# Kernel optimization log

Hardware: AMD Instinct MI355X
Metric: run time of the kernel (lower is better)

## Reference

```python
import jax, jax.numpy as jnp
import numpy as np

N, FDIM, HDIM, STEPS = 8192, 512, 1024, 50
STRESS, QNOISE = 0.0, 0.1


def setup_inputs() -> dict:
    key = jax.random.key(0)
    ks = jax.random.split(key, 20)
    s = 0.02
    d = {
        "real_antigen": jax.random.normal(ks[0], (N, FDIM), jnp.float32),
        "steps": STEPS,
        # quantum gene projection (self-loop graph -> per-node linear)
        "Wq": jax.random.normal(ks[1], (FDIM, HDIM), jnp.float32) * s,
        "bq": jnp.zeros((HDIM,), jnp.float32),
        # denoise_0: Linear(h,h) ReLU Linear(h,f)
        "W01": jax.random.normal(ks[2], (HDIM, HDIM), jnp.float32) * s,
        "b01": jnp.zeros((HDIM,), jnp.float32),
        "W02": jax.random.normal(ks[3], (HDIM, FDIM), jnp.float32) * s,
        "b02": jnp.zeros((FDIM,), jnp.float32),
        # denoise_1: Linear(h,h) Tanh Linear(h,f)
        "W11": jax.random.normal(ks[4], (HDIM, HDIM), jnp.float32) * s,
        "b11": jnp.zeros((HDIM,), jnp.float32),
        "W12": jax.random.normal(ks[5], (HDIM, FDIM), jnp.float32) * s,
        "b12": jnp.zeros((FDIM,), jnp.float32),
        # interference_net: Linear(2f,h) GELU Linear(h,f)
        "Wi1": jax.random.normal(ks[6], (2 * FDIM, HDIM), jnp.float32) * s,
        "bi1": jnp.zeros((HDIM,), jnp.float32),
        "Wi2": jax.random.normal(ks[7], (HDIM, FDIM), jnp.float32) * s,
        "bi2": jnp.zeros((FDIM,), jnp.float32),
        # quantum state scalars
        "alpha_amp": jnp.asarray(np.cos(0.6), jnp.float32),
        "beta_amp": jnp.asarray(np.sin(0.6), jnp.float32),
        "phase_cos": jnp.asarray(np.cos(0.3), jnp.float32),
    }
    return d


def reference(real_antigen, steps, Wq, bq, W01, b01, W02, b02, W11, b11,
              W12, b12, Wi1, bi1, Wi2, bi2, alpha_amp, beta_amp, phase_cos):
    sched = jnp.linspace(1e-4, 0.02, 100, dtype=jnp.float32)
    decoherence_rate = jnp.float32(0.1 + STRESS * 0.5)
    decay = jnp.exp(-decoherence_rate)
    # quantum probabilities (fixed amplitudes during the rollout)
    a2, b2 = alpha_amp ** 2, beta_amp ** 2
    p0 = a2 / (a2 + b2)
    p1 = b2 / (a2 + b2)
    sp0, sp1 = jnp.sqrt(p0), jnp.sqrt(p1)
    base_key = jax.random.key(1)
    x0 = jax.random.normal(jax.random.fold_in(base_key, 10_000), real_antigen.shape, jnp.float32)

    def step(carry, t):
        x, coh = carry
        qf = jax.nn.relu(x @ Wq + bq)                           # [N, H]
        d0 = jax.nn.relu(qf @ W01 + b01) @ W02 + b02            # [N, F]
        d1 = jnp.tanh(qf @ W11 + b11) @ W12 + b12               # [N, F]
        inter_in = jnp.concatenate([d0, d1], axis=-1)           # [N, 2F]
        interf = jax.nn.gelu(inter_in @ Wi1 + bi1, approximate=False) @ Wi2 + bi2
        qi = 2.0 * jnp.sqrt(p0 * p1) * phase_cos * coh          # scalar interference
        denoised = sp0 * d0 + sp1 * d1 + qi * interf
        alpha = jnp.maximum(1.0 - sched[t], 1e-8)
        alpha_prev = jnp.where(t > 0, 1.0 - sched[jnp.maximum(t - 1, 0)], 1.0)
        sqrt_1ma = jnp.sqrt(jnp.maximum(1.0 - alpha, 1e-8))
        x_new = (x - (1.0 - alpha) / sqrt_1ma * denoised) / jnp.sqrt(alpha)
        sigma = jnp.sqrt(jnp.maximum((1.0 - alpha_prev) / (1.0 - alpha) * (1.0 - alpha / alpha_prev), 0.0))
        noise = jax.random.normal(jax.random.fold_in(base_key, t), x.shape, jnp.float32)
        x_new = jnp.where(t > 0, x_new + (sigma + QNOISE * jnp.abs(qi)) * noise, x_new)
        return (x_new, coh * decay), None

    ts = jnp.arange(int(steps) - 1, -1, -1, dtype=jnp.int32)
    (x, _), _ = jax.lax.scan(step, (x0, jnp.float32(1.0)), ts)
    # quantum measurement: collapse to |0> with probability p0
    u = jax.random.uniform(jax.random.fold_in(base_key, 99_999), (), jnp.float32)
    dream = jnp.where(u < p0, 0.7 * x + 0.3 * real_antigen, x)
    return dream
```

## Files before the change

kernel.cpp:

```cpp
#include <hip/hip_runtime.h>
#include <stdint.h>
#include <math.h>


typedef __bf16 bf16x8 __attribute__((ext_vector_type(8)));
typedef float floatx4 __attribute__((ext_vector_type(4)));

__host__ __device__ inline void tf2x32(uint32_t k0, uint32_t k1,
                                       uint32_t x0, uint32_t x1,
                                       uint32_t& o0, uint32_t& o1) {
  uint32_t ks2 = k0 ^ k1 ^ 0x1BD11BDAu;
#define TF_R(r) { x0 += x1; x1 = (x1 << (r)) | (x1 >> (32 - (r))); x1 ^= x0; }
  x0 += k0; x1 += k1;
  TF_R(13) TF_R(15) TF_R(26) TF_R(6)
  x0 += k1;  x1 += ks2 + 1u;
  TF_R(17) TF_R(29) TF_R(16) TF_R(24)
  x0 += ks2; x1 += k0 + 2u;
  TF_R(13) TF_R(15) TF_R(26) TF_R(6)
  x0 += k0;  x1 += k1 + 3u;
  TF_R(17) TF_R(29) TF_R(16) TF_R(24)
  x0 += k1;  x1 += ks2 + 4u;
  TF_R(13) TF_R(15) TF_R(26) TF_R(6)
  x0 += ks2; x1 += k0 + 5u;
#undef TF_R
  o0 = x0; o1 = x1;
}

__device__ inline float erfinv_f32(float x) {
  float w = -log1pf(-x * x);
  float p;
  if (w < 5.0f) {
    w = w - 2.5f;
    p = 2.81022636e-08f;
    p = fmaf(p, w, 3.43273939e-07f);
    p = fmaf(p, w, -3.5233877e-06f);
    p = fmaf(p, w, -4.39150654e-06f);
    p = fmaf(p, w, 0.00021858087f);
    p = fmaf(p, w, -0.00125372503f);
    p = fmaf(p, w, -0.00417768164f);
    p = fmaf(p, w, 0.246640727f);
    p = fmaf(p, w, 1.50140941f);
  } else {
    w = sqrtf(w) - 3.0f;
    p = -0.000200214257f;
    p = fmaf(p, w, 0.000100950558f);
    p = fmaf(p, w, 0.00134934322f);
    p = fmaf(p, w, -0.00367342844f);
    p = fmaf(p, w, 0.00573950773f);
    p = fmaf(p, w, -0.0076224613f);
    p = fmaf(p, w, 0.00943887047f);
    p = fmaf(p, w, 1.00167406f);
    p = fmaf(p, w, 2.83297682f);
  }
  return p * x;
}

__device__ inline float tf_normal(uint32_t k0, uint32_t k1, uint32_t i) {
  uint32_t o0, o1;
  tf2x32(k0, k1, 0u, i, o0, o1);
  uint32_t bits = o0 ^ o1;
  float f = __uint_as_float(0x3F800000u | (bits >> 9)) - 1.0f;
  float u = f * 2.0f + (-0.99999994f);
  u = fmaxf(-0.99999994f, u);
  return 1.41421356f * erfinv_f32(u);
}

__device__ inline unsigned short f2bf(float f) {
  uint32_t u = __float_as_uint(f);
  u += 0x7FFFu + ((u >> 16) & 1u);
  return (unsigned short)(u >> 16);
}
__device__ inline float bf2f(unsigned short h) {
  return __uint_as_float(((uint32_t)h) << 16);
}

__global__ __launch_bounds__(256)
void transpose_bf16_kernel(const float* __restrict__ W,
                           unsigned short* __restrict__ Wt, int K, int N) {
  __shared__ float tile[32][33];
  int kb = blockIdx.x * 32, nb = blockIdx.y * 32;
  int tx = threadIdx.x & 31, ty = threadIdx.x >> 5;
#pragma unroll
  for (int i = 0; i < 32; i += 8)
    tile[ty + i][tx] = W[(size_t)(kb + ty + i) * N + nb + tx];
  __syncthreads();
#pragma unroll
  for (int i = 0; i < 32; i += 8)
    Wt[(size_t)(nb + ty + i) * K + kb + tx] = f2bf(tile[tx][ty + i]);
}

template<int MH, int NH>
__device__ __forceinline__ void phase_mfma8(bf16x8 (&a)[4][2], bf16x8 (&b)[4][2],
                                            floatx4 (&acc)[8][4]) {
  asm volatile("s_waitcnt lgkmcnt(0)" ::: "memory");
  __builtin_amdgcn_sched_barrier(0);
  __builtin_amdgcn_s_setprio(1);
#pragma unroll
  for (int s = 0; s < 2; s++)
#pragma unroll
    for (int mm = 0; mm < 4; mm++)
#pragma unroll
      for (int nn = 0; nn < 2; nn++)
        acc[MH * 4 + mm][NH * 2 + nn] = __builtin_amdgcn_mfma_f32_16x16x32_bf16(
            a[mm][s], b[NH * 2 + nn][s], acc[MH * 4 + mm][NH * 2 + nn], 0, 0, 0);
  __builtin_amdgcn_s_setprio(0);
}

template<int MH, int NH>
__device__ __forceinline__ void phase_mfma4(bf16x8 (&a)[4][2], bf16x8 (&b)[4][2],
                                            floatx4 (&acc)[4][4]) {
  asm volatile("s_waitcnt lgkmcnt(0)" ::: "memory");
  __builtin_amdgcn_sched_barrier(0);
  __builtin_amdgcn_s_setprio(1);
#pragma unroll
  for (int s = 0; s < 2; s++)
#pragma unroll
    for (int mm = 0; mm < 2; mm++)
#pragma unroll
      for (int nn = 0; nn < 2; nn++)
        acc[MH * 2 + mm][NH * 2 + nn] = __builtin_amdgcn_mfma_f32_16x16x32_bf16(
            a[MH * 2 + mm][s], b[NH * 2 + nn][s], acc[MH * 2 + mm][NH * 2 + nn],
            0, 0, 0);
  __builtin_amdgcn_s_setprio(0);
}

template<int ACT, int PAIR>
__global__ __launch_bounds__(512, 2)
void mfma_gemm_8ph_128x256(const unsigned short* __restrict__ A0,
                           const unsigned short* __restrict__ A1,
                           int lda0, int lda1, int K0, int Ktot,
                           const unsigned short* __restrict__ Bt,
                           const float* __restrict__ bias,
                           unsigned short* __restrict__ C, int ldc,
                           const unsigned short* __restrict__ Ab,
                           const unsigned short* __restrict__ Btb,
                           const float* __restrict__ biasb,
                           unsigned short* __restrict__ Cb) {
  __shared__ unsigned short As[2][128 * 64];
  __shared__ unsigned short Bs[2][256 * 64];
  const int tid = threadIdx.x;
  const int wave = tid >> 6, lane = tid & 63;
  const int wr = wave >> 2, wc = wave & 3;
  const int fm = lane & 15, quad = lane >> 4;
  const int id = blockIdx.x;
  const int nid = (id & 7) * 32 + (id >> 3);
  int row0, col0;
  if (PAIR) {
    const int rem = nid & 127;
    row0 = (rem & 63) << 7;
    col0 = (rem >> 6) << 8;
    if (nid >> 7) { A0 = Ab; A1 = Ab; Bt = Btb; bias = biasb; C = Cb; }
  } else {
    row0 = (nid & 63) << 7;
    col0 = (nid >> 6) << 8;
  }
  const int NKT = Ktot >> 6;

  auto stageA = [&](int tile, int buf, int h) {
    if (tile >= NKT) return;
    const int kk = tile << 6;
    const unsigned short* Ap; int kOff, lda;
    if (kk < K0) { Ap = A0; kOff = kk; lda = lda0; }
    else         { Ap = A1; kOff = kk - K0; lda = lda1; }
    const int sr = tid >> 3, gc = tid & 7;
    __builtin_amdgcn_global_load_lds(
        (const __attribute__((address_space(1))) uint32_t*)
            (Ap + (size_t)(row0 + h * 64 + sr) * lda + kOff + ((gc ^ (sr & 7)) << 3)),
        (__attribute__((address_space(3))) uint32_t*)(&As[buf][h * 4096 + tid * 8]),
        16, 0, 0);
  };
  auto stageB = [&](int tile, int buf, int h) {
    if (tile >= NKT) return;
    const int kk = tile << 6;
#pragma unroll
    for (int c = 0; c < 2; c++) {
      int g2 = c * 512 + tid;
      int sr = g2 >> 3, gc = g2 & 7;
      __builtin_amdgcn_global_load_lds(
          (const __attribute__((address_space(1))) uint32_t*)
              (Bt + (size_t)(col0 + h * 128 + sr) * Ktot + kk + ((gc ^ (sr & 7)) << 3)),
          (__attribute__((address_space(3))) uint32_t*)(&Bs[buf][h * 8192 + g2 * 8]),
          16, 0, 0);
    }
  };

  const int aswz = (fm & 7) << 3;
  auto rdA = [&](int buf, int m, int s) {
    return *(const bf16x8*)(&As[buf][(wr * 64 + m * 16 + fm) * 64 +
                                     ((s * 32 + quad * 8) ^ aswz)]);
  };
  auto rdB = [&](int buf, int n, int s) {
    return *(const bf16x8*)(&Bs[buf][(wc * 64 + n * 16 + fm) * 64 +
                                     ((s * 32 + quad * 8) ^ aswz)]);
  };

  floatx4 acc[4][4];
#pragma unroll
  for (int m = 0; m < 4; m++)
#pragma unroll
    for (int n = 0; n < 4; n++) acc[m][n] = (floatx4){0.f, 0.f, 0.f, 0.f};

  stageA(0, 0, 0); stageA(0, 0, 1);
  stageB(0, 0, 0); stageB(0, 0, 1);
  stageB(1, 1, 0); stageB(1, 1, 1);
  asm volatile("s_waitcnt vmcnt(4)" ::: "memory");
  asm volatile("s_barrier" ::: "memory");

  const int NJ = NKT >> 1;
#pragma unroll 1
  for (int j = 0; j < NJ; j++) {
    const int t1 = 2 * j + 1;
    bf16x8 a[4][2], b[4][2];
#pragma unroll
    for (int mm = 0; mm < 2; mm++) { a[mm][0] = rdA(0, mm, 0); a[mm][1] = rdA(0, mm, 1); }
#pragma unroll
    for (int nn = 0; nn < 2; nn++) { b[nn][0] = rdB(0, nn, 0); b[nn][1] = rdB(0, nn, 1); }
    stageA(t1, 1, 0);
    asm volatile("s_barrier" ::: "memory");
    phase_mfma4<0, 0>(a, b, acc);
    asm volatile("s_barrier" ::: "memory");
#pragma unroll
    for (int nn = 2; nn < 4; nn++) { b[nn][0] = rdB(0, nn, 0); b[nn][1] = rdB(0, nn, 1); }
    stageA(t1, 1, 1);
    asm volatile("s_barrier" ::: "memory");
    phase_mfma4<0, 1>(a, b, acc);
    asm volatile("s_barrier" ::: "memory");
#pragma unroll
    for (int mm = 2; mm < 4; mm++) { a[mm][0] = rdA(0, mm, 0); a[mm][1] = rdA(0, mm, 1); }
    stageB(t1 + 1, 0, 0);
    asm volatile("s_barrier" ::: "memory");
    phase_mfma4<1, 1>(a, b, acc);
    asm volatile("s_barrier" ::: "memory");
    stageB(t1 + 1, 0, 1);
    asm volatile("s_barrier" ::: "memory");
    phase_mfma4<1, 0>(a, b, acc);
    if (j == NJ - 1) asm volatile("s_waitcnt vmcnt(0)" ::: "memory");
    else             asm volatile("s_waitcnt vmcnt(4)" ::: "memory");
    asm volatile("s_barrier" ::: "memory");
#pragma unroll
    for (int mm = 0; mm < 2; mm++) { a[mm][0] = rdA(1, mm, 0); a[mm][1] = rdA(1, mm, 1); }
#pragma unroll
    for (int nn = 0; nn < 2; nn++) { b[nn][0] = rdB(1, nn, 0); b[nn][1] = rdB(1, nn, 1); }
    stageA(t1 + 1, 0, 0);
    asm volatile("s_barrier" ::: "memory");
    phase_mfma4<0, 0>(a, b, acc);
    asm volatile("s_barrier" ::: "memory");
#pragma unroll
    for (int nn = 2; nn < 4; nn++) { b[nn][0] = rdB(1, nn, 0); b[nn][1] = rdB(1, nn, 1); }
    stageA(t1 + 1, 0, 1);
    asm volatile("s_barrier" ::: "memory");
    phase_mfma4<0, 1>(a, b, acc);
    asm volatile("s_barrier" ::: "memory");
#pragma unroll
    for (int mm = 2; mm < 4; mm++) { a[mm][0] = rdA(1, mm, 0); a[mm][1] = rdA(1, mm, 1); }
    stageB(t1 + 2, 1, 0);
    asm volatile("s_barrier" ::: "memory");
    phase_mfma4<1, 1>(a, b, acc);
    asm volatile("s_barrier" ::: "memory");
    stageB(t1 + 2, 1, 1);
    asm volatile("s_barrier" ::: "memory");
    phase_mfma4<1, 0>(a, b, acc);
    asm volatile("s_waitcnt vmcnt(4)" ::: "memory");
    asm volatile("s_barrier" ::: "memory");
  }

#pragma unroll
  for (int n = 0; n < 4; n++) {
    int col = col0 + wc * 64 + n * 16 + fm;
    float bv = bias[col];
#pragma unroll
    for (int m = 0; m < 4; m++) {
      int rbase = row0 + wr * 64 + m * 16 + quad * 4;
#pragma unroll
      for (int r = 0; r < 4; r++) {
        float val = acc[m][n][r] + bv;
        if (ACT == 1) val = fmaxf(val, 0.0f);
        if (ACT == 3) val = 0.5f * val * (1.0f + erff(val * 0.70710678118654752f));
        C[(size_t)(rbase + r) * ldc + col] = f2bf(val);
      }
    }
  }
}

__global__ __launch_bounds__(512, 2)
void mfma_gemm2_8ph(const unsigned short* __restrict__ A,
                    const unsigned short* __restrict__ Bt,
                    const float* __restrict__ bias0,
                    const float* __restrict__ bias1,
                    unsigned short* __restrict__ C0,
                    unsigned short* __restrict__ C1) {
  constexpr int NKT = 16;
  __shared__ unsigned short As[2][256 * 64];
  __shared__ unsigned short Bs[2][256 * 64];
  const int tid = threadIdx.x;
  const int wave = tid >> 6, lane = tid & 63;
  const int wr = wave >> 2, wc = wave & 3;
  const int fm = lane & 15, quad = lane >> 4;
  const int id = blockIdx.x;
  const int nid = (id & 7) * 32 + (id >> 3);
  const int row0 = (nid & 31) << 8;
  const int col0 = (nid >> 5) << 8;

  auto stageA = [&](int tile, int buf, int h) {
    if (tile >= NKT) return;
    const int kk = tile << 6;
#pragma unroll
    for (int c = 0; c < 2; c++) {
      int g2 = c * 512 + tid;
      int sr = g2 >> 3, gc = g2 & 7;
      __builtin_amdgcn_global_load_lds(
          (const __attribute__((address_space(1))) uint32_t*)
              (A + (size_t)(row0 + h * 128 + sr) * 1024 + kk + ((gc ^ (sr & 7)) << 3)),
          (__attribute__((address_space(3))) uint32_t*)(&As[buf][h * 8192 + g2 * 8]),
          16, 0, 0);
    }
  };
  auto stageB = [&](int tile, int buf, int h) {
    if (tile >= NKT) return;
    const int kk = tile << 6;
#pragma unroll
    for (int c = 0; c < 2; c++) {
      int g2 = c * 512 + tid;
      int sr = g2 >> 3, gc = g2 & 7;
      __builtin_amdgcn_global_load_lds(
          (const __attribute__((address_space(1))) uint32_t*)
              (Bt + (size_t)(col0 + h * 128 + sr) * 1024 + kk + ((gc ^ (sr & 7)) << 3)),
          (__attribute__((address_space(3))) uint32_t*)(&Bs[buf][h * 8192 + g2 * 8]),
          16, 0, 0);
    }
  };

  const int aswz = (fm & 7) << 3;
  auto rdA = [&](int buf, int m, int s) {
    return *(const bf16x8*)(&As[buf][(wr * 128 + m * 16 + fm) * 64 +
                                     ((s * 32 + quad * 8) ^ aswz)]);
  };
  auto rdB = [&](int buf, int n, int s) {
    return *(const bf16x8*)(&Bs[buf][(wc * 64 + n * 16 + fm) * 64 +
                                     ((s * 32 + quad * 8) ^ aswz)]);
  };

  floatx4 acc[8][4];
#pragma unroll
  for (int m = 0; m < 8; m++)
#pragma unroll
    for (int n = 0; n < 4; n++) acc[m][n] = (floatx4){0.f, 0.f, 0.f, 0.f};

  stageA(0, 0, 0); stageA(0, 0, 1);
  stageB(0, 0, 0); stageB(0, 0, 1);
  stageB(1, 1, 0); stageB(1, 1, 1);
  asm volatile("s_waitcnt vmcnt(4)" ::: "memory");
  asm volatile("s_barrier" ::: "memory");

#pragma unroll 1
  for (int j = 0; j < 8; j++) {
    const int t1 = 2 * j + 1;
    bf16x8 a[4][2], b[4][2];
#pragma unroll
    for (int mm = 0; mm < 4; mm++) { a[mm][0] = rdA(0, mm, 0); a[mm][1] = rdA(0, mm, 1); }
#pragma unroll
    for (int nn = 0; nn < 2; nn++) { b[nn][0] = rdB(0, nn, 0); b[nn][1] = rdB(0, nn, 1); }
    stageA(t1, 1, 0);
    asm volatile("s_barrier" ::: "memory");
    phase_mfma8<0, 0>(a, b, acc);
    asm volatile("s_barrier" ::: "memory");
#pragma unroll
    for (int nn = 2; nn < 4; nn++) { b[nn][0] = rdB(0, nn, 0); b[nn][1] = rdB(0, nn, 1); }
    stageA(t1, 1, 1);
    asm volatile("s_barrier" ::: "memory");
    phase_mfma8<0, 1>(a, b, acc);
    asm volatile("s_barrier" ::: "memory");
#pragma unroll
    for (int mm = 0; mm < 4; mm++) { a[mm][0] = rdA(0, 4 + mm, 0); a[mm][1] = rdA(0, 4 + mm, 1); }
    stageB(t1 + 1, 0, 0);
    asm volatile("s_barrier" ::: "memory");
    phase_mfma8<1, 1>(a, b, acc);
    asm volatile("s_barrier" ::: "memory");
    stageB(t1 + 1, 0, 1);
    asm volatile("s_barrier" ::: "memory");
    phase_mfma8<1, 0>(a, b, acc);
    if (j == 7) asm volatile("s_waitcnt vmcnt(0)" ::: "memory");
    else        asm volatile("s_waitcnt vmcnt(4)" ::: "memory");
    asm volatile("s_barrier" ::: "memory");
#pragma unroll
    for (int mm = 0; mm < 4; mm++) { a[mm][0] = rdA(1, mm, 0); a[mm][1] = rdA(1, mm, 1); }
#pragma unroll
    for (int nn = 0; nn < 2; nn++) { b[nn][0] = rdB(1, nn, 0); b[nn][1] = rdB(1, nn, 1); }
    stageA(t1 + 1, 0, 0);
    asm volatile("s_barrier" ::: "memory");
    phase_mfma8<0, 0>(a, b, acc);
    asm volatile("s_barrier" ::: "memory");
#pragma unroll
    for (int nn = 2; nn < 4; nn++) { b[nn][0] = rdB(1, nn, 0); b[nn][1] = rdB(1, nn, 1); }
    stageA(t1 + 1, 0, 1);
    asm volatile("s_barrier" ::: "memory");
    phase_mfma8<0, 1>(a, b, acc);
    asm volatile("s_barrier" ::: "memory");
#pragma unroll
    for (int mm = 0; mm < 4; mm++) { a[mm][0] = rdA(1, 4 + mm, 0); a[mm][1] = rdA(1, 4 + mm, 1); }
    stageB(t1 + 2, 1, 0);
    asm volatile("s_barrier" ::: "memory");
    phase_mfma8<1, 1>(a, b, acc);
    asm volatile("s_barrier" ::: "memory");
    stageB(t1 + 2, 1, 1);
    asm volatile("s_barrier" ::: "memory");
    phase_mfma8<1, 0>(a, b, acc);
    asm volatile("s_waitcnt vmcnt(4)" ::: "memory");
    asm volatile("s_barrier" ::: "memory");
  }

  const bool side = (col0 >= 1024);
  const float* bias = side ? bias1 : bias0;
  unsigned short* C = side ? C1 : C0;
  const int cb = col0 - (side ? 1024 : 0);
#pragma unroll
  for (int n = 0; n < 4; n++) {
    int col = cb + wc * 64 + n * 16 + fm;
    float bv = bias[col];
#pragma unroll
    for (int m = 0; m < 8; m++) {
      int rbase = row0 + wr * 128 + m * 16 + quad * 4;
#pragma unroll
      for (int r = 0; r < 4; r++) {
        float val = acc[m][n][r] + bv;
        val = side ? tanhf(val) : fmaxf(val, 0.0f);
        C[(size_t)(rbase + r) * 1024 + col] = f2bf(val);
      }
    }
  }
}

__global__ __launch_bounds__(512, 4)
void mfma_gemm_update(const unsigned short* __restrict__ A,
                      const unsigned short* __restrict__ Bt,
                      const float* __restrict__ bias,
                      const unsigned short* __restrict__ d0,
                      const unsigned short* __restrict__ d1,
                      float* __restrict__ x,
                      unsigned short* __restrict__ xbf,
                      const float* __restrict__ a_amp,
                      const float* __restrict__ b_amp,
                      const float* __restrict__ ph,
                      float coh, float c1, float sqa, float sigma,
                      int add_noise, uint32_t k0, uint32_t k1) {
  __shared__ unsigned short As[2][64 * 32];
  __shared__ unsigned short Bs[2][128 * 32];
  const int tid = threadIdx.x;
  const int wave = tid >> 6, lane = tid & 63;
  const int wr = wave >> 2, wc = wave & 3;
  const int fm = lane & 15, quad = lane >> 4;
  const int id = blockIdx.x + gridDim.x * blockIdx.y;
  const int row0 = (id & 127) << 6;
  const int col0 = (id >> 7) << 7;
  const int sArow = (tid & 255) >> 2;
  const int sBrow = tid >> 2;
  const int sgr = (tid & 3) * 8;

  auto issue = [&](int kt, int buf) {
    const int kk = kt * 32;
    __builtin_amdgcn_global_load_lds(
        (const __attribute__((address_space(1))) uint32_t*)
            (A + (size_t)(row0 + sArow) * 1024 + kk + sgr),
        (__attribute__((address_space(3))) uint32_t*)(&As[buf][sArow * 32 + sgr]),
        16, 0, 0);
    __builtin_amdgcn_global_load_lds(
        (const __attribute__((address_space(1))) uint32_t*)
            (Bt + (size_t)(col0 + sBrow) * 1024 + kk + sgr),
        (__attribute__((address_space(3))) uint32_t*)(&Bs[buf][sBrow * 32 + sgr]),
        16, 0, 0);
  };

  floatx4 acc[2][2];
#pragma unroll
  for (int tm = 0; tm < 2; tm++)
#pragma unroll
    for (int tn = 0; tn < 2; tn++) acc[tm][tn] = (floatx4){0.f, 0.f, 0.f, 0.f};

  const int nk = 32;
  issue(0, 0);
  for (int k = 0; k < nk; k++) {
    const int cur = k & 1;
    if (k + 1 < nk) {
      issue(k + 1, cur ^ 1);
      asm volatile("s_waitcnt vmcnt(2)\ns_barrier" ::: "memory");
    } else {
      asm volatile("s_waitcnt vmcnt(0)\ns_barrier" ::: "memory");
    }
    bf16x8 a[2], b[2];
#pragma unroll
    for (int tm = 0; tm < 2; tm++)
      a[tm] = *(const bf16x8*)(&As[cur][(wr * 32 + tm * 16 + fm) * 32 + quad * 8]);
#pragma unroll
    for (int tn = 0; tn < 2; tn++)
      b[tn] = *(const bf16x8*)(&Bs[cur][(wc * 32 + tn * 16 + fm) * 32 + quad * 8]);
#pragma unroll
    for (int tm = 0; tm < 2; tm++)
#pragma unroll
      for (int tn = 0; tn < 2; tn++)
        acc[tm][tn] = __builtin_amdgcn_mfma_f32_16x16x32_bf16(a[tm], b[tn],
                                                              acc[tm][tn], 0, 0, 0);
    asm volatile("s_barrier" ::: "memory");
  }

  float aa = a_amp[0], bb = b_amp[0], pc = ph[0];
  float a2 = aa * aa, b2 = bb * bb, s = a2 + b2;
  float p0 = a2 / s, p1 = b2 / s;
  float sp0 = sqrtf(p0), sp1 = sqrtf(p1);
  float qi = 2.0f * sqrtf(p0 * p1) * pc * coh;
  float nscale = sigma + 0.1f * fabsf(qi);

#pragma unroll
  for (int tn = 0; tn < 2; tn++) {
    int col = col0 + wc * 32 + tn * 16 + fm;
    float bv = bias[col];
#pragma unroll
    for (int tm = 0; tm < 2; tm++) {
      int rbase = row0 + wr * 32 + tm * 16 + quad * 4;
#pragma unroll
      for (int r = 0; r < 4; r++) {
        int row = rbase + r;
        size_t i = (size_t)row * 512 + col;
        float itf = acc[tm][tn][r] + bv;
        float den = sp0 * bf2f(d0[i]) + sp1 * bf2f(d1[i]) + qi * itf;
        float xn = (x[i] - c1 * den) / sqa;
        if (add_noise) xn += nscale * tf_normal(k0, k1, (uint32_t)i);
        x[i] = xn;
        xbf[i] = f2bf(xn);
      }
    }
  }
}

__global__ void init_normal_kernel(float* __restrict__ x,
                                   unsigned short* __restrict__ xbf,
                                   uint32_t k0, uint32_t k1, int n) {
  int i = blockIdx.x * blockDim.x + threadIdx.x;
  if (i >= n) return;
  float v = tf_normal(k0, k1, (uint32_t)i);
  x[i] = v;
  xbf[i] = f2bf(v);
}

__global__ void final_kernel(const float* __restrict__ x,
                             const float* __restrict__ real,
                             float* __restrict__ out,
                             const float* __restrict__ a_amp,
                             const float* __restrict__ b_amp,
                             uint32_t k0, uint32_t k1, int n) {
  int i = blockIdx.x * blockDim.x + threadIdx.x;
  if (i >= n) return;
  float aa = a_amp[0], bb = b_amp[0];
  float a2 = aa * aa, b2 = bb * bb;
  float p0 = a2 / (a2 + b2);
  uint32_t o0, o1;
  tf2x32(k0, k1, 0u, 0u, o0, o1);
  uint32_t bits = o0 ^ o1;
  float u = __uint_as_float(0x3F800000u | (bits >> 9)) - 1.0f;
  float xv = x[i];
  out[i] = (u < p0) ? (0.7f * xv + 0.3f * real[i]) : xv;
}

extern "C" void kernel_launch(void* const* d_in, const int* in_sizes, int n_in,
                              void* d_out, int out_size, void* d_ws,
                              size_t ws_size, hipStream_t stream) {
  const float* real = (const float*)d_in[0];
  const float* Wq  = (const float*)d_in[2];
  const float* bq  = (const float*)d_in[3];
  const float* W01 = (const float*)d_in[4];
  const float* b01 = (const float*)d_in[5];
  const float* W02 = (const float*)d_in[6];
  const float* b02 = (const float*)d_in[7];
  const float* W11 = (const float*)d_in[8];
  const float* b11 = (const float*)d_in[9];
  const float* W12 = (const float*)d_in[10];
  const float* b12 = (const float*)d_in[11];
  const float* Wi1 = (const float*)d_in[12];
  const float* bi1 = (const float*)d_in[13];
  const float* Wi2 = (const float*)d_in[14];
  const float* bi2 = (const float*)d_in[15];
  const float* a_amp = (const float*)d_in[16];
  const float* b_amp = (const float*)d_in[17];
  const float* ph    = (const float*)d_in[18];

  const int Nn = 8192, F = 512, H = 1024;
  const int nElem = Nn * F;

  char* ws = (char*)d_ws;
  float* x = (float*)ws;                                   ws += (size_t)nElem * 4;
  unsigned short* xbf = (unsigned short*)ws;               ws += (size_t)nElem * 2;
  unsigned short* qf  = (unsigned short*)ws;               ws += (size_t)Nn * H * 2;
  unsigned short* h0  = (unsigned short*)ws;               ws += (size_t)Nn * H * 2;
  unsigned short* h1  = (unsigned short*)ws;               ws += (size_t)Nn * H * 2;
  unsigned short* d0  = (unsigned short*)ws;               ws += (size_t)nElem * 2;
  unsigned short* d1  = (unsigned short*)ws;               ws += (size_t)nElem * 2;
  unsigned short* Wq_t  = (unsigned short*)ws;             ws += (size_t)F * H * 2;
  unsigned short* WA_t  = (unsigned short*)ws;             ws += (size_t)(2 * H) * H * 2;
  unsigned short* W02_t = (unsigned short*)ws;             ws += (size_t)H * F * 2;
  unsigned short* W12_t = (unsigned short*)ws;             ws += (size_t)H * F * 2;
  unsigned short* Wi1_t = (unsigned short*)ws;             ws += (size_t)(2 * F) * H * 2;
  unsigned short* Wi2_t = (unsigned short*)ws;             ws += (size_t)H * F * 2;

  dim3 tb(256);
  transpose_bf16_kernel<<<dim3(F / 32, H / 32), tb, 0, stream>>>(Wq, Wq_t, F, H);
  transpose_bf16_kernel<<<dim3(H / 32, H / 32), tb, 0, stream>>>(W01, WA_t, H, H);
  transpose_bf16_kernel<<<dim3(H / 32, H / 32), tb, 0, stream>>>(W11, WA_t + (size_t)H * H, H, H);
  transpose_bf16_kernel<<<dim3(H / 32, F / 32), tb, 0, stream>>>(W02, W02_t, H, F);
  transpose_bf16_kernel<<<dim3(H / 32, F / 32), tb, 0, stream>>>(W12, W12_t, H, F);
  transpose_bf16_kernel<<<dim3(2 * F / 32, H / 32), tb, 0, stream>>>(Wi1, Wi1_t, 2 * F, H);
  transpose_bf16_kernel<<<dim3(H / 32, F / 32), tb, 0, stream>>>(Wi2, Wi2_t, H, F);

  uint32_t kx0, kx1; tf2x32(0u, 1u, 0u, 10000u, kx0, kx1);
  init_normal_kernel<<<(nElem + 255) / 256, 256, 0, stream>>>(x, xbf, kx0, kx1, nElem);

  float sched[100];
  for (int i = 0; i < 100; i++)
    sched[i] = (float)(1e-4 + (0.02 - 1e-4) * (double)i / 99.0);
  const float decay = expf(-0.1f);
  float coh = 1.0f;

  dim3 blk(512);
  dim3 g8(256);
  dim3 g7(F / 128, Nn / 64);

  for (int j = 0; j < 50; j++) {
    int t = 49 - j;
    mfma_gemm_8ph_128x256<1, 0><<<g8, blk, 0, stream>>>(
        xbf, xbf, F, F, F, F, Wq_t, bq, qf, H,
        nullptr, nullptr, nullptr, nullptr);
    mfma_gemm2_8ph<<<g8, blk, 0, stream>>>(qf, WA_t, b01, b11, h0, h1);
    mfma_gemm_8ph_128x256<0, 1><<<g8, blk, 0, stream>>>(
        h0, h0, H, H, H, H, W02_t, b02, d0, F,
        h1, W12_t, b12, d1);
    mfma_gemm_8ph_128x256<3, 0><<<g8, blk, 0, stream>>>(
        d0, d1, F, F, F, 2 * F, Wi1_t, bi1, qf, H,
        nullptr, nullptr, nullptr, nullptr);

    float schedt = sched[t];
    float alphaf = fmaxf(1.0f - schedt, 1e-8f);
    float one_m_alpha = 1.0f - alphaf;
    float sqrt_1ma = sqrtf(fmaxf(one_m_alpha, 1e-8f));
    float c1 = one_m_alpha / sqrt_1ma;
    float sqa = sqrtf(alphaf);
    float sigma = 0.0f;
    if (t > 0) {
      float ap = 1.0f - sched[t - 1];
      sigma = sqrtf(fmaxf((1.0f - ap) / one_m_alpha * (1.0f - alphaf / ap), 0.0f));
    }
    uint32_t kt0, kt1; tf2x32(0u, 1u, 0u, (uint32_t)t, kt0, kt1);
    mfma_gemm_update<<<g7, blk, 0, stream>>>(
        qf, Wi2_t, bi2, d0, d1, x, xbf, a_amp, b_amp, ph, coh, c1, sqa, sigma,
        (t > 0) ? 1 : 0, kt0, kt1);
    coh *= decay;
  }

  uint32_t ku0, ku1; tf2x32(0u, 1u, 0u, 99999u, ku0, ku1);
  final_kernel<<<(nElem + 255) / 256, 256, 0, stream>>>(
      x, real, (float*)d_out, a_amp, b_amp, ku0, ku1, nElem);
}
```

Measured before the change: 8.053 ms.

## Shrink generic GEMM tile to 128x128 with 512 blocks; batch weight transposes

The generic 8-phase MFMA GEMM goes from a 128x256 to a 128x128 output tile. Each wave now holds a 4x2 accumulator set, the B staging buffer is halved, and launch bounds allow 4 blocks per CU. The grid doubles to 512 blocks so the three GEMMs using this kernel fill the 256 CUs more evenly and can hide latency with higher occupancy, at the cost of less B-operand reuse per block and more A re-reads. The seven weight-transpose launches are also merged into one batched kernel indexed by blockIdx.z, which cuts launch overhead in setup.

```diff
diff --git a/kernel.cpp b/kernel.cpp
--- a/kernel.cpp
+++ b/kernel.cpp
@@ -74,11 +74,22 @@
   return __uint_as_float(((uint32_t)h) << 16);
 }
 
+struct TPBatch {
+  const float* W[7];
+  unsigned short* Wt[7];
+  int K[7];
+  int N[7];
+};
+
 __global__ __launch_bounds__(256)
-void transpose_bf16_kernel(const float* __restrict__ W,
-                           unsigned short* __restrict__ Wt, int K, int N) {
+void transpose_bf16_batched(TPBatch tp) {
+  const int z = blockIdx.z;
+  const int K = tp.K[z], N = tp.N[z];
+  const int kb = blockIdx.x * 32, nb = blockIdx.y * 32;
+  if (kb >= K || nb >= N) return;
+  const float* __restrict__ W = tp.W[z];
+  unsigned short* __restrict__ Wt = tp.Wt[z];
   __shared__ float tile[32][33];
-  int kb = blockIdx.x * 32, nb = blockIdx.y * 32;
   int tx = threadIdx.x & 31, ty = threadIdx.x >> 5;
 #pragma unroll
   for (int i = 0; i < 32; i += 8)
@@ -107,8 +118,8 @@
 }
 
 template<int MH, int NH>
-__device__ __forceinline__ void phase_mfma4(bf16x8 (&a)[4][2], bf16x8 (&b)[4][2],
-                                            floatx4 (&acc)[4][4]) {
+__device__ __forceinline__ void phase_mfma2(bf16x8 (&a)[4][2], bf16x8 (&b)[2][2],
+                                            floatx4 (&acc)[4][2]) {
   asm volatile("s_waitcnt lgkmcnt(0)" ::: "memory");
   __builtin_amdgcn_sched_barrier(0);
   __builtin_amdgcn_s_setprio(1);
@@ -116,17 +127,14 @@
   for (int s = 0; s < 2; s++)
 #pragma unroll
     for (int mm = 0; mm < 2; mm++)
-#pragma unroll
-      for (int nn = 0; nn < 2; nn++)
-        acc[MH * 2 + mm][NH * 2 + nn] = __builtin_amdgcn_mfma_f32_16x16x32_bf16(
-            a[MH * 2 + mm][s], b[NH * 2 + nn][s], acc[MH * 2 + mm][NH * 2 + nn],
-            0, 0, 0);
+      acc[MH * 2 + mm][NH] = __builtin_amdgcn_mfma_f32_16x16x32_bf16(
+          a[MH * 2 + mm][s], b[NH][s], acc[MH * 2 + mm][NH], 0, 0, 0);
   __builtin_amdgcn_s_setprio(0);
 }
 
 template<int ACT, int PAIR>
-__global__ __launch_bounds__(512, 2)
-void mfma_gemm_8ph_128x256(const unsigned short* __restrict__ A0,
+__global__ __launch_bounds__(512, 4)
+void mfma_gemm_8ph_128x128(const unsigned short* __restrict__ A0,
                            const unsigned short* __restrict__ A1,
                            int lda0, int lda1, int K0, int Ktot,
                            const unsigned short* __restrict__ Bt,
@@ -137,22 +145,22 @@
                            const float* __restrict__ biasb,
                            unsigned short* __restrict__ Cb) {
   __shared__ unsigned short As[2][128 * 64];
-  __shared__ unsigned short Bs[2][256 * 64];
+  __shared__ unsigned short Bs[2][128 * 64];
   const int tid = threadIdx.x;
   const int wave = tid >> 6, lane = tid & 63;
   const int wr = wave >> 2, wc = wave & 3;
   const int fm = lane & 15, quad = lane >> 4;
   const int id = blockIdx.x;
-  const int nid = (id & 7) * 32 + (id >> 3);
+  const int nid = (id & 7) * 64 + (id >> 3);
   int row0, col0;
   if (PAIR) {
-    const int rem = nid & 127;
+    const int rem = nid & 255;
     row0 = (rem & 63) << 7;
-    col0 = (rem >> 6) << 8;
-    if (nid >> 7) { A0 = Ab; A1 = Ab; Bt = Btb; bias = biasb; C = Cb; }
+    col0 = (rem >> 6) << 7;
+    if (nid >> 8) { A0 = Ab; A1 = Ab; Bt = Btb; bias = biasb; C = Cb; }
   } else {
     row0 = (nid & 63) << 7;
-    col0 = (nid >> 6) << 8;
+    col0 = (nid >> 6) << 7;
   }
   const int NKT = Ktot >> 6;
 
@@ -172,16 +180,12 @@
   auto stageB = [&](int tile, int buf, int h) {
     if (tile >= NKT) return;
     const int kk = tile << 6;
-#pragma unroll
-    for (int c = 0; c < 2; c++) {
-      int g2 = c * 512 + tid;
-      int sr = g2 >> 3, gc = g2 & 7;
-      __builtin_amdgcn_global_load_lds(
-          (const __attribute__((address_space(1))) uint32_t*)
-              (Bt + (size_t)(col0 + h * 128 + sr) * Ktot + kk + ((gc ^ (sr & 7)) << 3)),
-          (__attribute__((address_space(3))) uint32_t*)(&Bs[buf][h * 8192 + g2 * 8]),
-          16, 0, 0);
-    }
+    const int sr = tid >> 3, gc = tid & 7;
+    __builtin_amdgcn_global_load_lds(
+        (const __attribute__((address_space(1))) uint32_t*)
+            (Bt + (size_t)(col0 + h * 64 + sr) * Ktot + kk + ((gc ^ (sr & 7)) << 3)),
+        (__attribute__((address_space(3))) uint32_t*)(&Bs[buf][h * 4096 + tid * 8]),
+        16, 0, 0);
   };
 
   const int aswz = (fm & 7) << 3;
@@ -190,83 +194,79 @@
                                      ((s * 32 + quad * 8) ^ aswz)]);
   };
   auto rdB = [&](int buf, int n, int s) {
-    return *(const bf16x8*)(&Bs[buf][(wc * 64 + n * 16 + fm) * 64 +
+    return *(const bf16x8*)(&Bs[buf][(wc * 32 + n * 16 + fm) * 64 +
                                      ((s * 32 + quad * 8) ^ aswz)]);
   };
 
-  floatx4 acc[4][4];
+  floatx4 acc[4][2];
 #pragma unroll
   for (int m = 0; m < 4; m++)
 #pragma unroll
-    for (int n = 0; n < 4; n++) acc[m][n] = (floatx4){0.f, 0.f, 0.f, 0.f};
+    for (int n = 0; n < 2; n++) acc[m][n] = (floatx4){0.f, 0.f, 0.f, 0.f};
 
   stageA(0, 0, 0); stageA(0, 0, 1);
   stageB(0, 0, 0); stageB(0, 0, 1);
   stageB(1, 1, 0); stageB(1, 1, 1);
-  asm volatile("s_waitcnt vmcnt(4)" ::: "memory");
+  asm volatile("s_waitcnt vmcnt(2)" ::: "memory");
   asm volatile("s_barrier" ::: "memory");
 
   const int NJ = NKT >> 1;
 #pragma unroll 1
   for (int j = 0; j < NJ; j++) {
     const int t1 = 2 * j + 1;
-    bf16x8 a[4][2], b[4][2];
+    bf16x8 a[4][2], b[2][2];
 #pragma unroll
     for (int mm = 0; mm < 2; mm++) { a[mm][0] = rdA(0, mm, 0); a[mm][1] = rdA(0, mm, 1); }
-#pragma unroll
-    for (int nn = 0; nn < 2; nn++) { b[nn][0] = rdB(0, nn, 0); b[nn][1] = rdB(0, nn, 1); }
+    b[0][0] = rdB(0, 0, 0); b[0][1] = rdB(0, 0, 1);
     stageA(t1, 1, 0);
     asm volatile("s_barrier" ::: "memory");
-    phase_mfma4<0, 0>(a, b, acc);
-    asm volatile("s_barrier" ::: "memory");
-#pragma unroll
-    for (int nn = 2; nn < 4; nn++) { b[nn][0] = rdB(0, nn, 0); b[nn][1] = rdB(0, nn, 1); }
+    phase_mfma2<0, 0>(a, b, acc);
+    asm volatile("s_barrier" ::: "memory");
+    b[1][0] = rdB(0, 1, 0); b[1][1] = rdB(0, 1, 1);
     stageA(t1, 1, 1);
     asm volatile("s_barrier" ::: "memory");
-    phase_mfma4<0, 1>(a, b, acc);
+    phase_mfma2<0, 1>(a, b, acc);
     asm volatile("s_barrier" ::: "memory");
 #pragma unroll
     for (int mm = 2; mm < 4; mm++) { a[mm][0] = rdA(0, mm, 0); a[mm][1] = rdA(0, mm, 1); }
     stageB(t1 + 1, 0, 0);
     asm volatile("s_barrier" ::: "memory");
-    phase_mfma4<1, 1>(a, b, acc);
+    phase_mfma2<1, 1>(a, b, acc);
     asm volatile("s_barrier" ::: "memory");
     stageB(t1 + 1, 0, 1);
     asm volatile("s_barrier" ::: "memory");
-    phase_mfma4<1, 0>(a, b, acc);
+    phase_mfma2<1, 0>(a, b, acc);
     if (j == NJ - 1) asm volatile("s_waitcnt vmcnt(0)" ::: "memory");
-    else             asm volatile("s_waitcnt vmcnt(4)" ::: "memory");
+    else             asm volatile("s_waitcnt vmcnt(2)" ::: "memory");
     asm volatile("s_barrier" ::: "memory");
 #pragma unroll
     for (int mm = 0; mm < 2; mm++) { a[mm][0] = rdA(1, mm, 0); a[mm][1] = rdA(1, mm, 1); }
-#pragma unroll
-    for (int nn = 0; nn < 2; nn++) { b[nn][0] = rdB(1, nn, 0); b[nn][1] = rdB(1, nn, 1); }
+    b[0][0] = rdB(1, 0, 0); b[0][1] = rdB(1, 0, 1);
     stageA(t1 + 1, 0, 0);
     asm volatile("s_barrier" ::: "memory");
-    phase_mfma4<0, 0>(a, b, acc);
-    asm volatile("s_barrier" ::: "memory");
-#pragma unroll
-    for (int nn = 2; nn < 4; nn++) { b[nn][0] = rdB(1, nn, 0); b[nn][1] = rdB(1, nn, 1); }
+    phase_mfma2<0, 0>(a, b, acc);
+    asm volatile("s_barrier" ::: "memory");
+    b[1][0] = rdB(1, 1, 0); b[1][1] = rdB(1, 1, 1);
     stageA(t1 + 1, 0, 1);
     asm volatile("s_barrier" ::: "memory");
-    phase_mfma4<0, 1>(a, b, acc);
+    phase_mfma2<0, 1>(a, b, acc);
     asm volatile("s_barrier" ::: "memory");
 #pragma unroll
     for (int mm = 2; mm < 4; mm++) { a[mm][0] = rdA(1, mm, 0); a[mm][1] = rdA(1, mm, 1); }
     stageB(t1 + 2, 1, 0);
     asm volatile("s_barrier" ::: "memory");
-    phase_mfma4<1, 1>(a, b, acc);
+    phase_mfma2<1, 1>(a, b, acc);
     asm volatile("s_barrier" ::: "memory");
     stageB(t1 + 2, 1, 1);
     asm volatile("s_barrier" ::: "memory");
-    phase_mfma4<1, 0>(a, b, acc);
-    asm volatile("s_waitcnt vmcnt(4)" ::: "memory");
-    asm volatile("s_barrier" ::: "memory");
-  }
-
-#pragma unroll
-  for (int n = 0; n < 4; n++) {
-    int col = col0 + wc * 64 + n * 16 + fm;
+    phase_mfma2<1, 0>(a, b, acc);
+    asm volatile("s_waitcnt vmcnt(2)" ::: "memory");
+    asm volatile("s_barrier" ::: "memory");
+  }
+
+#pragma unroll
+  for (int n = 0; n < 2; n++) {
+    int col = col0 + wc * 32 + n * 16 + fm;
     float bv = bias[col];
 #pragma unroll
     for (int m = 0; m < 4; m++) {
@@ -600,14 +600,15 @@
   unsigned short* Wi1_t = (unsigned short*)ws;             ws += (size_t)(2 * F) * H * 2;
   unsigned short* Wi2_t = (unsigned short*)ws;             ws += (size_t)H * F * 2;
 
-  dim3 tb(256);
-  transpose_bf16_kernel<<<dim3(F / 32, H / 32), tb, 0, stream>>>(Wq, Wq_t, F, H);
-  transpose_bf16_kernel<<<dim3(H / 32, H / 32), tb, 0, stream>>>(W01, WA_t, H, H);
-  transpose_bf16_kernel<<<dim3(H / 32, H / 32), tb, 0, stream>>>(W11, WA_t + (size_t)H * H, H, H);
-  transpose_bf16_kernel<<<dim3(H / 32, F / 32), tb, 0, stream>>>(W02, W02_t, H, F);
-  transpose_bf16_kernel<<<dim3(H / 32, F / 32), tb, 0, stream>>>(W12, W12_t, H, F);
-  transpose_bf16_kernel<<<dim3(2 * F / 32, H / 32), tb, 0, stream>>>(Wi1, Wi1_t, 2 * F, H);
-  transpose_bf16_kernel<<<dim3(H / 32, F / 32), tb, 0, stream>>>(Wi2, Wi2_t, H, F);
+  TPBatch tp;
+  tp.W[0] = Wq;  tp.Wt[0] = Wq_t;                  tp.K[0] = F;     tp.N[0] = H;
+  tp.W[1] = W01; tp.Wt[1] = WA_t;                  tp.K[1] = H;     tp.N[1] = H;
+  tp.W[2] = W11; tp.Wt[2] = WA_t + (size_t)H * H;  tp.K[2] = H;     tp.N[2] = H;
+  tp.W[3] = W02; tp.Wt[3] = W02_t;                 tp.K[3] = H;     tp.N[3] = F;
+  tp.W[4] = W12; tp.Wt[4] = W12_t;                 tp.K[4] = H;     tp.N[4] = F;
+  tp.W[5] = Wi1; tp.Wt[5] = Wi1_t;                 tp.K[5] = 2 * F; tp.N[5] = H;
+  tp.W[6] = Wi2; tp.Wt[6] = Wi2_t;                 tp.K[6] = H;     tp.N[6] = F;
+  transpose_bf16_batched<<<dim3(32, 32, 7), dim3(256), 0, stream>>>(tp);
 
   uint32_t kx0, kx1; tf2x32(0u, 1u, 0u, 10000u, kx0, kx1);
   init_normal_kernel<<<(nElem + 255) / 256, 256, 0, stream>>>(x, xbf, kx0, kx1, nElem);
@@ -619,19 +620,20 @@
   float coh = 1.0f;
 
   dim3 blk(512);
-  dim3 g8(256);
+  dim3 g2(256);
+  dim3 g512(512);
   dim3 g7(F / 128, Nn / 64);
 
   for (int j = 0; j < 50; j++) {
     int t = 49 - j;
-    mfma_gemm_8ph_128x256<1, 0><<<g8, blk, 0, stream>>>(
+    mfma_gemm_8ph_128x128<1, 0><<<g512, blk, 0, stream>>>(
         xbf, xbf, F, F, F, F, Wq_t, bq, qf, H,
         nullptr, nullptr, nullptr, nullptr);
-    mfma_gemm2_8ph<<<g8, blk, 0, stream>>>(qf, WA_t, b01, b11, h0, h1);
-    mfma_gemm_8ph_128x256<0, 1><<<g8, blk, 0, stream>>>(
+    mfma_gemm2_8ph<<<g2, blk, 0, stream>>>(qf, WA_t, b01, b11, h0, h1);
+    mfma_gemm_8ph_128x128<0, 1><<<g512, blk, 0, stream>>>(
         h0, h0, H, H, H, H, W02_t, b02, d0, F,
         h1, W12_t, b12, d1);
-    mfma_gemm_8ph_128x256<3, 0><<<g8, blk, 0, stream>>>(
+    mfma_gemm_8ph_128x128<3, 0><<<g512, blk, 0, stream>>>(
         d0, d1, F, F, F, 2 * F, Wi1_t, bi1, qf, H,
         nullptr, nullptr, nullptr, nullptr);
 
```

Result: no change. 8.110 ms (+0.7%).
